# Performance work log

Hardware: AMD Instinct MI355X
Metric: run time of the kernel (lower is better)

The kernel has to match this reference:

```python
import jax, jax.numpy as jnp
import numpy as np

TEMPERATURE = 0.5


def setup_inputs() -> dict:
    key = jax.random.key(0)
    k1, k2 = jax.random.split(key)
    B, D = 4096, 256
    emb_i = jax.random.normal(k1, (B, D), dtype=jnp.float32)
    emb_j = jax.random.normal(k2, (B, D), dtype=jnp.float32)
    return {"emb_i": emb_i, "emb_j": emb_j}


def reference(emb_i, emb_j):
    B = emb_i.shape[0]
    # L2-normalize along feature dim (torch F.normalize uses eps=1e-12 clamp)
    def l2norm(x):
        n = jnp.sqrt(jnp.sum(x * x, axis=1, keepdims=True))
        return x / jnp.maximum(n, 1e-12)

    z_i = l2norm(emb_i)
    z_j = l2norm(emb_j)
    reps = jnp.concatenate([z_i, z_j], axis=0)  # [2B, D]
    # cosine similarity of normalized rows == plain GEMM
    sim = (reps @ reps.T) / TEMPERATURE  # [2B, 2B]
    # mask out self-similarity on the diagonal
    diag = jnp.eye(2 * B, dtype=bool)
    sim = jnp.where(diag, -jnp.inf, sim)
    # labels: row i -> i+B, row B+i -> i
    labels = jnp.concatenate([jnp.arange(B) + B, jnp.arange(B)])
    logp = jax.nn.log_softmax(sim, axis=1)
    loss = -jnp.mean(jnp.take_along_axis(logp, labels[:, None], axis=1))
    return loss
```

## Files before the change

kernel.cpp:

```cpp
#include <hip/hip_runtime.h>

typedef __bf16 bf16x8 __attribute__((ext_vector_type(8)));
typedef float f32x4 __attribute__((ext_vector_type(4)));

#define D_DIM 256
#define INV_T 2.0f

__device__ __forceinline__ unsigned short f2bf(float f) {
  union { float f; unsigned u; } x; x.f = f;
  unsigned r = x.u + 0x7FFFu + ((x.u >> 16) & 1u);
  return (unsigned short)(r >> 16);
}

__global__ __launch_bounds__(256) void k_normalize(const float* __restrict__ ei,
                                                   const float* __restrict__ ej,
                                                   unsigned short* __restrict__ R,
                                                   unsigned* __restrict__ ticket,
                                                   int B) {
  if (blockIdx.x == 0 && threadIdx.x == 0) *ticket = 0u;
  const int w = threadIdx.x >> 6, lane = threadIdx.x & 63;
  const int row = blockIdx.x * 4 + w;
  const float* src = (row < B) ? (ei + (size_t)row * D_DIM)
                               : (ej + (size_t)(row - B) * D_DIM);
  float4 v = reinterpret_cast<const float4*>(src)[lane];
  float ss = v.x * v.x + v.y * v.y + v.z * v.z + v.w * v.w;
#pragma unroll
  for (int d = 32; d; d >>= 1) ss += __shfl_xor(ss, d, 64);
  float s = 1.0f / fmaxf(sqrtf(ss), 1e-12f);
  ushort4 o;
  o.x = f2bf(v.x * s); o.y = f2bf(v.y * s);
  o.z = f2bf(v.z * s); o.w = f2bf(v.w * s);
  reinterpret_cast<ushort4*>(R + (size_t)row * D_DIM)[lane] = o;
}

__global__ __launch_bounds__(256, 4) void k_simgemm(const unsigned short* __restrict__ R,
                                                    float* __restrict__ rowPartial,
                                                    float* __restrict__ simTgt,
                                                    int N) {
  __shared__ char lds[32 * 1024];
  const int tid = threadIdx.x;
  const int w = tid >> 6, lane = tid & 63;
  const int wr = w >> 1, wc = w & 1;
  const int half = N >> 1;

  const int T = N / 128;
  const int t = blockIdx.x;
  int bi = (int)(((float)(2 * T + 1) -
                  sqrtf((float)((2 * T + 1) * (2 * T + 1) - 8 * t))) * 0.5f);
  while (bi > 0 && t < bi * (2 * T - bi + 1) / 2) --bi;
  while (t >= (bi + 1) * (2 * T - bi) / 2) ++bi;
  const int bj = bi + (t - bi * (2 * T - bi + 1) / 2);
  const int brow = bi * 128, bcol = bj * 128;
  const bool offdiag = (bi != bj);

  f32x4 zero4 = {0.f, 0.f, 0.f, 0.f};
  f32x4 acc[4][4];
#pragma unroll
  for (int m = 0; m < 4; ++m)
#pragma unroll
    for (int n = 0; n < 4; ++n) acc[m][n] = zero4;

  auto stage = [&](int kt) {
    char* ldsA = lds;
    char* ldsB = lds + 16 * 1024;
#pragma unroll
    for (int i = 0; i < 4; ++i) {
      const int grp = i * 4 + w;
      const int c = grp * 64 + lane;
      const int r = c >> 3, j = c & 7;
      const int k8 = j ^ (r & 7);
      const unsigned short* gA = R + (size_t)(brow + r) * D_DIM + kt * 64 + k8 * 8;
      const unsigned short* gB = R + (size_t)(bcol + r) * D_DIM + kt * 64 + k8 * 8;
      __builtin_amdgcn_global_load_lds(
          (const __attribute__((address_space(1))) void*)gA,
          (__attribute__((address_space(3))) void*)(ldsA + (size_t)grp * 1024), 16, 0, 0);
      __builtin_amdgcn_global_load_lds(
          (const __attribute__((address_space(1))) void*)gB,
          (__attribute__((address_space(3))) void*)(ldsB + (size_t)grp * 1024), 16, 0, 0);
    }
  };

  auto compute = [&]() {
    const char* ldsA = lds;
    const char* ldsB = lds + 16 * 1024;
#pragma unroll
    for (int kk = 0; kk < 2; ++kk) {
      const int k8 = kk * 4 + (lane >> 4);
      bf16x8 a[4], b[4];
#pragma unroll
      for (int m = 0; m < 4; ++m) {
        const int row = wr * 64 + m * 16 + (lane & 15);
        a[m] = *reinterpret_cast<const bf16x8*>(ldsA + (row * 8 + (k8 ^ (row & 7))) * 16);
      }
#pragma unroll
      for (int n = 0; n < 4; ++n) {
        const int col = wc * 64 + n * 16 + (lane & 15);
        b[n] = *reinterpret_cast<const bf16x8*>(ldsB + (col * 8 + (k8 ^ (col & 7))) * 16);
      }
#pragma unroll
      for (int m = 0; m < 4; ++m)
#pragma unroll
        for (int n = 0; n < 4; ++n)
          acc[m][n] = __builtin_amdgcn_mfma_f32_16x16x32_bf16(a[m], b[n], acc[m][n], 0, 0, 0);
    }
  };

#pragma unroll
  for (int kt = 0; kt < 4; ++kt) {
    stage(kt);
    __syncthreads();
    compute();
    __syncthreads();
  }

  float cs[4] = {0.f, 0.f, 0.f, 0.f};
#pragma unroll
  for (int m = 0; m < 4; ++m) {
#pragma unroll
    for (int j = 0; j < 4; ++j) {
      const int gr = brow + wr * 64 + m * 16 + (lane >> 4) * 4 + j;
      const int tgt = (gr < half) ? gr + half : gr - half;
      float rs = 0.f;
#pragma unroll
      for (int n = 0; n < 4; ++n) {
        const int gc = bcol + wc * 64 + n * 16 + (lane & 15);
        const float sv = acc[m][n][j] * INV_T;
        const float ev = (gr == gc) ? 0.f : __expf(sv);
        if (gc == tgt) {
          simTgt[gr] = sv;
          if (offdiag) simTgt[gc] = sv;
        }
        rs += ev;
        cs[n] += ev;
      }
#pragma unroll
      for (int d = 1; d < 16; d <<= 1) rs += __shfl_xor(rs, d, 64);
      if ((lane & 15) == 0)
        rowPartial[(size_t)(bj * 2 + wc) * N + gr] = rs;
    }
  }
  if (offdiag) {
#pragma unroll
    for (int n = 0; n < 4; ++n) {
      float c = cs[n];
      c += __shfl_xor(c, 16, 64);
      c += __shfl_xor(c, 32, 64);
      if ((lane >> 4) == 0)
        rowPartial[(size_t)(bi * 2 + wr) * N + (bcol + wc * 64 + n * 16 + lane)] = c;
    }
  }
}

__global__ __launch_bounds__(256) void k_rowreduce(const float* __restrict__ rowPartial,
                                                   const float* __restrict__ simTgt,
                                                   float* __restrict__ blockOut,
                                                   unsigned* __restrict__ ticket,
                                                   float* __restrict__ out, int N) {
  const int row = blockIdx.x * 256 + threadIdx.x;
  float denom = 0.f;
#pragma unroll 8
  for (int c = 0; c < 128; ++c) denom += rowPartial[(size_t)c * N + row];
  float lossr = __logf(denom) - simTgt[row];
#pragma unroll
  for (int d = 32; d; d >>= 1) lossr += __shfl_xor(lossr, d, 64);
  __shared__ float red[4];
  __shared__ int isLast;
  if ((threadIdx.x & 63) == 0) red[threadIdx.x >> 6] = lossr;
  __syncthreads();
  if (threadIdx.x == 0) {
    atomicExch(&blockOut[blockIdx.x], red[0] + red[1] + red[2] + red[3]);
    isLast = (atomicAdd(ticket, 1u) == gridDim.x - 1);
  }
  __syncthreads();
  if (isLast && threadIdx.x < 64) {
    float v = (threadIdx.x < gridDim.x) ? atomicAdd(&blockOut[threadIdx.x], 0.0f) : 0.f;
#pragma unroll
    for (int d = 32; d; d >>= 1) v += __shfl_xor(v, d, 64);
    if (threadIdx.x == 0) out[0] = v / (float)N;
  }
}

extern "C" void kernel_launch(void* const* d_in, const int* in_sizes, int n_in,
                              void* d_out, int out_size, void* d_ws, size_t ws_size,
                              hipStream_t stream) {
  const float* ei = (const float*)d_in[0];
  const float* ej = (const float*)d_in[1];
  const int B = in_sizes[0] / D_DIM;
  const int N = 2 * B;

  char* ws = (char*)d_ws;
  unsigned short* R = (unsigned short*)ws;
  float* rowPartial = (float*)(ws + (size_t)N * D_DIM * 2);
  float* simTgt     = (float*)(ws + (size_t)N * D_DIM * 2 + (size_t)128 * N * 4);
  float* blockOut   = (float*)((char*)simTgt + (size_t)N * 4);
  unsigned* ticket  = (unsigned*)((char*)blockOut + (size_t)(N / 256) * 4);

  k_normalize<<<N / 4, 256, 0, stream>>>(ei, ej, R, ticket, B);
  const int T = N / 128;
  k_simgemm<<<T * (T + 1) / 2, 256, 0, stream>>>(R, rowPartial, simTgt, N);
  k_rowreduce<<<N / 256, 256, 0, stream>>>(rowPartial, simTgt, blockOut, ticket,
                                           (float*)d_out, N);
}
```

Measured before the change: 53.38 us.

## Double-buffer GEMM K-loop with async LDS loads and use exp2/log2 epilogue

```diff
diff --git a/kernel.cpp b/kernel.cpp
--- a/kernel.cpp
+++ b/kernel.cpp
@@ -4,7 +4,8 @@
 typedef float f32x4 __attribute__((ext_vector_type(4)));
 
 #define D_DIM 256
-#define INV_T 2.0f
+#define C2 2.88539008f
+#define LN2 0.69314718f
 
 __device__ __forceinline__ unsigned short f2bf(float f) {
   union { float f; unsigned u; } x; x.f = f;
@@ -37,7 +38,7 @@
                                                     float* __restrict__ rowPartial,
                                                     float* __restrict__ simTgt,
                                                     int N) {
-  __shared__ char lds[32 * 1024];
+  __shared__ char lds[2][16 * 1024];
   const int tid = threadIdx.x;
   const int w = tid >> 6, lane = tid & 63;
   const int wr = w >> 1, wc = w & 1;
@@ -60,57 +61,57 @@
 #pragma unroll
     for (int n = 0; n < 4; ++n) acc[m][n] = zero4;
 
-  auto stage = [&](int kt) {
-    char* ldsA = lds;
-    char* ldsB = lds + 16 * 1024;
+  auto stage = [&](int buf, int kt) {
+    char* dst = lds[buf];
 #pragma unroll
     for (int i = 0; i < 4; ++i) {
       const int grp = i * 4 + w;
-      const int c = grp * 64 + lane;
-      const int r = c >> 3, j = c & 7;
-      const int k8 = j ^ (r & 7);
-      const unsigned short* gA = R + (size_t)(brow + r) * D_DIM + kt * 64 + k8 * 8;
-      const unsigned short* gB = R + (size_t)(bcol + r) * D_DIM + kt * 64 + k8 * 8;
+      const int cp = (grp & 7) * 64 + lane;
+      const int r = cp >> 2, js = cp & 3;
+      const int j = js ^ ((r >> 1) & 3);
+      const int base = (grp < 8) ? brow : bcol;
+      const unsigned short* g = R + (size_t)(base + r) * D_DIM + kt * 32 + j * 8;
       __builtin_amdgcn_global_load_lds(
-          (const __attribute__((address_space(1))) void*)gA,
-          (__attribute__((address_space(3))) void*)(ldsA + (size_t)grp * 1024), 16, 0, 0);
-      __builtin_amdgcn_global_load_lds(
-          (const __attribute__((address_space(1))) void*)gB,
-          (__attribute__((address_space(3))) void*)(ldsB + (size_t)grp * 1024), 16, 0, 0);
+          (const __attribute__((address_space(1))) void*)g,
+          (__attribute__((address_space(3))) void*)(dst + (size_t)grp * 1024), 16, 0, 0);
     }
   };
 
-  auto compute = [&]() {
-    const char* ldsA = lds;
-    const char* ldsB = lds + 16 * 1024;
-#pragma unroll
-    for (int kk = 0; kk < 2; ++kk) {
-      const int k8 = kk * 4 + (lane >> 4);
-      bf16x8 a[4], b[4];
-#pragma unroll
-      for (int m = 0; m < 4; ++m) {
-        const int row = wr * 64 + m * 16 + (lane & 15);
-        a[m] = *reinterpret_cast<const bf16x8*>(ldsA + (row * 8 + (k8 ^ (row & 7))) * 16);
-      }
-#pragma unroll
-      for (int n = 0; n < 4; ++n) {
-        const int col = wc * 64 + n * 16 + (lane & 15);
-        b[n] = *reinterpret_cast<const bf16x8*>(ldsB + (col * 8 + (k8 ^ (col & 7))) * 16);
-      }
-#pragma unroll
-      for (int m = 0; m < 4; ++m)
-#pragma unroll
-        for (int n = 0; n < 4; ++n)
-          acc[m][n] = __builtin_amdgcn_mfma_f32_16x16x32_bf16(a[m], b[n], acc[m][n], 0, 0, 0);
-    }
+  auto compute = [&](int buf) {
+    const char* ldsA = lds[buf];
+    const char* ldsB = lds[buf] + 8 * 1024;
+    const int k8 = lane >> 4;
+    bf16x8 a[4], b[4];
+#pragma unroll
+    for (int m = 0; m < 4; ++m) {
+      const int row = wr * 64 + m * 16 + (lane & 15);
+      a[m] = *reinterpret_cast<const bf16x8*>(ldsA + (row * 4 + (k8 ^ ((row >> 1) & 3))) * 16);
+    }
+#pragma unroll
+    for (int n = 0; n < 4; ++n) {
+      const int col = wc * 64 + n * 16 + (lane & 15);
+      b[n] = *reinterpret_cast<const bf16x8*>(ldsB + (col * 4 + (k8 ^ ((col >> 1) & 3))) * 16);
+    }
+#pragma unroll
+    for (int m = 0; m < 4; ++m)
+#pragma unroll
+      for (int n = 0; n < 4; ++n)
+        acc[m][n] = __builtin_amdgcn_mfma_f32_16x16x32_bf16(a[m], b[n], acc[m][n], 0, 0, 0);
   };
 
-#pragma unroll
-  for (int kt = 0; kt < 4; ++kt) {
-    stage(kt);
-    __syncthreads();
-    compute();
-    __syncthreads();
+  stage(0, 0);
+#pragma unroll
+  for (int kt = 0; kt < 8; ++kt) {
+    const int cur = kt & 1;
+    if (kt < 7) {
+      stage(cur ^ 1, kt + 1);
+      asm volatile("s_waitcnt vmcnt(4)" ::: "memory");
+    } else {
+      asm volatile("s_waitcnt vmcnt(0)" ::: "memory");
+    }
+    __builtin_amdgcn_s_barrier();
+    compute(cur);
+    __builtin_amdgcn_s_barrier();
   }
 
   float cs[4] = {0.f, 0.f, 0.f, 0.f};
@@ -124,11 +125,11 @@
 #pragma unroll
       for (int n = 0; n < 4; ++n) {
         const int gc = bcol + wc * 64 + n * 16 + (lane & 15);
-        const float sv = acc[m][n][j] * INV_T;
-        const float ev = (gr == gc) ? 0.f : __expf(sv);
+        const float sv2 = acc[m][n][j] * C2;
+        const float ev = (gr == gc) ? 0.f : __builtin_amdgcn_exp2f(sv2);
         if (gc == tgt) {
-          simTgt[gr] = sv;
-          if (offdiag) simTgt[gc] = sv;
+          simTgt[gr] = sv2;
+          if (offdiag) simTgt[gc] = sv2;
         }
         rs += ev;
         cs[n] += ev;
@@ -160,7 +161,7 @@
   float denom = 0.f;
 #pragma unroll 8
   for (int c = 0; c < 128; ++c) denom += rowPartial[(size_t)c * N + row];
-  float lossr = __logf(denom) - simTgt[row];
+  float lossr = (__builtin_amdgcn_logf(denom) - simTgt[row]) * LN2;
 #pragma unroll
   for (int d = 32; d; d >>= 1) lossr += __shfl_xor(lossr, d, 64);
   __shared__ float red[4];
```

Result: faster. 49.09 us (-8.0%).
